# Kernel optimization log

Measured on AMD Instinct MI355X. Metric: run time of the kernel, lower is better.

The kernel has to match this reference:

```python
import jax, jax.numpy as jnp
import numpy as np

NUM_EXPERTS = 8
NUM_LANGS = 4
TOP_K = 2
D_MODEL = 1024
EXPERT_SIZE = 4096
B, S = 2, 2048


def setup_inputs() -> dict:
    key = jax.random.key(0)
    ks = jax.random.split(key, 6)
    def xavier(k, shape, fan_in, fan_out):
        a = float(np.sqrt(6.0 / (fan_in + fan_out)))
        return jax.random.uniform(k, shape, jnp.float32, -a, a)
    return {
        "x": jax.random.normal(ks[0], (B, S, D_MODEL), jnp.float32),
        "router_w": xavier(ks[1], (NUM_EXPERTS, D_MODEL), D_MODEL, NUM_EXPERTS),
        "router_b": jnp.zeros((NUM_EXPERTS,), jnp.float32),
        "lang_w": xavier(ks[2], (NUM_LANGS, D_MODEL), D_MODEL, NUM_LANGS),
        "lang_b": jnp.zeros((NUM_LANGS,), jnp.float32),
        "w1": xavier(ks[3], (NUM_EXPERTS, D_MODEL, EXPERT_SIZE), D_MODEL, EXPERT_SIZE),
        "b1": jnp.zeros((NUM_EXPERTS, EXPERT_SIZE), jnp.float32),
        "w2": xavier(ks[4], (NUM_EXPERTS, EXPERT_SIZE, D_MODEL), EXPERT_SIZE, D_MODEL),
        "b2": jnp.zeros((NUM_EXPERTS, D_MODEL), jnp.float32),
    }


def reference(x, router_w, router_b, lang_w, lang_b, w1, b1, w2, b2):
    # Language-aware routing bias
    lang_logits = x @ lang_w.T + lang_b                      # [B,S,L]
    lang_probs = jax.nn.softmax(lang_logits, axis=-1)
    # lang_probs[..., idx:idx+2].sum(-1): slice may be width 1 at the edge,
    # emulate with a zero pad column.
    lp_pad = jnp.pad(lang_probs, ((0, 0), (0, 0), (0, 1)))
    idx = jnp.arange(NUM_EXPERTS) % NUM_LANGS                # [E]
    expert_weights = lp_pad[..., idx] + lp_pad[..., idx + 1] # [B,S,E]

    router_logits = x @ router_w.T + router_b + 0.1 * expert_weights
    router_probs = jax.nn.softmax(router_logits, axis=-1)   # [B,S,E]
    top_p, top_i = jax.lax.top_k(router_probs, TOP_K)        # [B,S,K]
    top_p = top_p / top_p.sum(axis=-1, keepdims=True)

    # Dense per-expert MLP (dropout=0 / eval). torch GELU default = exact erf.
    h = jax.nn.gelu(jnp.einsum('bsd,edh->bseh', x, w1) + b1, approximate=False)
    expert_out = jnp.einsum('bseh,ehd->bsed', h, w2) + b2    # [B,S,E,D]

    sel = jnp.take_along_axis(expert_out, top_i[..., None], axis=2)  # [B,S,K,D]
    return (top_p[..., None] * sel).sum(axis=2)              # [B,S,D]
```

## Files before the change

### kernel.cpp

```cpp
#include <hip/hip_runtime.h>
#include <cstdint>
#include <cstddef>

#define T_TOK 4096
#define DM 1024
#define HS 4096
#define NE 8
#define MAXROWS 9216
#define MAXTILES 72

typedef __attribute__((ext_vector_type(8))) short short8;
typedef __attribute__((ext_vector_type(4))) float floatx4;

__device__ __forceinline__ unsigned short f2bf(float f) {
  union { float f; unsigned u; } v; v.f = f;
  unsigned r = (v.u + 0x7fffu + ((v.u >> 16) & 1u)) >> 16;
  return (unsigned short)r;
}

__device__ __forceinline__ void gload_lds16(const void* g, void* l) {
  __builtin_amdgcn_global_load_lds((const __attribute__((address_space(1))) void*)g,
                                   (__attribute__((address_space(3))) void*)l, 16, 0, 0);
}


__global__ void k_init(int* counts, int* cursor, unsigned* list) {
  int i = blockIdx.x * 256 + threadIdx.x;
  if (i < NE) { counts[i] = 0; cursor[i] = 0; }
  if (i < MAXROWS) list[i] = 0xFFFFFFFFu;
}

__global__ void k_route(const float* __restrict__ x, const float* __restrict__ rw,
                        const float* __restrict__ rb, const float* __restrict__ lw,
                        const float* __restrict__ lb, int* __restrict__ top_i,
                        float* __restrict__ top_p, int* __restrict__ counts) {
  int t = blockIdx.x * 4 + (threadIdx.x >> 6);
  int lane = threadIdx.x & 63;
  const float4* xt = (const float4*)(x + (size_t)t * DM);
  float4 xv[4];
#pragma unroll
  for (int j = 0; j < 4; j++) xv[j] = xt[lane * 4 + j];
  float dots[12];
#pragma unroll
  for (int r = 0; r < 12; r++) {
    const float4* wr = (const float4*)(r < 4 ? lw + r * DM : rw + (r - 4) * DM);
    float s = 0.f;
#pragma unroll
    for (int j = 0; j < 4; j++) {
      float4 w = wr[lane * 4 + j];
      s += xv[j].x * w.x + xv[j].y * w.y + xv[j].z * w.z + xv[j].w * w.w;
    }
#pragma unroll
    for (int o = 32; o > 0; o >>= 1) s += __shfl_xor(s, o, 64);
    dots[r] = s;
  }
  if (lane == 0) {
    float lp[4]; float m = -1e30f;
#pragma unroll
    for (int i = 0; i < 4; i++) { lp[i] = dots[i] + lb[i]; m = fmaxf(m, lp[i]); }
    float sum = 0.f;
#pragma unroll
    for (int i = 0; i < 4; i++) { lp[i] = expf(lp[i] - m); sum += lp[i]; }
#pragma unroll
    for (int i = 0; i < 4; i++) lp[i] /= sum;
    float ew[4];
    ew[0] = lp[0] + lp[1]; ew[1] = lp[1] + lp[2]; ew[2] = lp[2] + lp[3]; ew[3] = lp[3];
    float r8[8];
#pragma unroll
    for (int e = 0; e < 8; e++) r8[e] = dots[4 + e] + rb[e] + 0.1f * ew[e & 3];
    int e0 = 0;
#pragma unroll
    for (int e = 1; e < 8; e++) if (r8[e] > r8[e0]) e0 = e;
    int e1 = (e0 == 0) ? 1 : 0;
#pragma unroll
    for (int e = 0; e < 8; e++) if (e != e0 && r8[e] > r8[e1]) e1 = e;
    float tt = expf(r8[e1] - r8[e0]);
    float w0 = 1.f / (1.f + tt);
    float w1 = tt / (1.f + tt);
    top_i[t * 2] = e0; top_i[t * 2 + 1] = e1;
    top_p[t * 2] = w0; top_p[t * 2 + 1] = w1;
    atomicAdd(&counts[e0], 1); atomicAdd(&counts[e1], 1);
  }
}

__global__ void k_offsets(const int* counts, int* off) {
  if (threadIdx.x == 0) {
    int acc = 0;
    for (int e = 0; e < NE; e++) {
      off[e] = acc;
      int p = ((counts[e] + 127) >> 7) << 7;
      acc += p;
    }
    off[NE] = acc;
  }
}

__global__ void k_scatter(const int* __restrict__ top_i, const int* __restrict__ off,
                          int* cursor, unsigned* __restrict__ list) {
  int t = blockIdx.x * 256 + threadIdx.x;
  if (t >= T_TOK) return;
#pragma unroll
  for (int k = 0; k < 2; k++) {
    int e = top_i[t * 2 + k];
    int pos = atomicAdd(&cursor[e], 1);
    list[off[e] + pos] = (unsigned)(t * 2 + k);
  }
}

__global__ void k_cvt_x(const float* __restrict__ x, unsigned short* __restrict__ xb) {
  int i = blockIdx.x * 256 + threadIdx.x;
  float4 v = ((const float4*)x)[i];
  union { unsigned short us[4]; uint2 u2; } o;
  o.us[0] = f2bf(v.x); o.us[1] = f2bf(v.y); o.us[2] = f2bf(v.z); o.us[3] = f2bf(v.w);
  ((uint2*)xb)[i] = o.u2;
}

__global__ void k_transpose_bf16(const float* __restrict__ src, unsigned short* __restrict__ dst,
                                 int K, int N) {
  __shared__ float tile[64][65];
  const float* s = src + (size_t)blockIdx.z * K * N;
  unsigned short* d = dst + (size_t)blockIdx.z * K * N;
  int n0 = blockIdx.x * 64, k0 = blockIdx.y * 64;
  int tr = threadIdx.x >> 4;
  int tc = (threadIdx.x & 15) * 4;
#pragma unroll
  for (int j = 0; j < 4; j++) {
    int row = tr + j * 16;
    float4 v = *(const float4*)&s[(size_t)(k0 + row) * N + n0 + tc];
    tile[row][tc + 0] = v.x; tile[row][tc + 1] = v.y;
    tile[row][tc + 2] = v.z; tile[row][tc + 3] = v.w;
  }
  __syncthreads();
#pragma unroll
  for (int j = 0; j < 4; j++) {
    int n = tr + j * 16;
    union { unsigned short us[4]; uint2 u2; } o;
#pragma unroll
    for (int i = 0; i < 4; i++) o.us[i] = f2bf(tile[tc + i][n]);
    *(uint2*)&d[(size_t)(n0 + n) * K + k0 + tc] = o.u2;
  }
}

__global__ void k_init_out(const int* __restrict__ top_i, const float* __restrict__ top_p,
                           const float* __restrict__ b2, float* __restrict__ out) {
  int i = blockIdx.x * 256 + threadIdx.x;
  int t = i >> 10, d = i & 1023;
  int e0 = top_i[t * 2], e1 = top_i[t * 2 + 1];
  out[i] = top_p[t * 2] * b2[e0 * DM + d] + top_p[t * 2 + 1] * b2[e1 * DM + d];
}

template <int MODE>
__global__ __launch_bounds__(256, 4) void k_gemm(
    const unsigned short* __restrict__ Abase,
    const unsigned short* __restrict__ Wt,
    const int* __restrict__ off, const unsigned* __restrict__ list,
    const float* __restrict__ b1, const float* __restrict__ top_p,
    unsigned short* __restrict__ Hout, float* __restrict__ out,
    int K, int N) {
  int nx = gridDim.x;
  int flat = blockIdx.y * nx + blockIdx.x;
  int cpx = (nx * gridDim.y) >> 3;
  int swz = (flat & 7) * cpx + (flat >> 3);
  int n0 = (swz % nx) * 128;
  int r0 = (swz / nx) * 128;

  int total = off[NE];
  if (r0 >= total) return;
  int e = 0;
  while (r0 >= off[e + 1]) ++e;

  __shared__ __align__(16) unsigned short lA[2][128 * 32];
  __shared__ __align__(16) unsigned short lB[2][128 * 32];
  __shared__ float sP[128];
  __shared__ int sTok[128];

  int tid = threadIdx.x;
  int srow = tid >> 2;
  int key_s = (srow >> 1) & 3;
  int koff_src = (((tid & 3) ^ key_s) * 8);
  int kdst = (tid & 3) * 8;

  const unsigned short* srcA[2];
#pragma unroll
  for (int c = 0; c < 2; c++) {
    int row = c * 64 + srow;
    size_t arow;
    if (MODE == 0) {
      unsigned pair = list[r0 + row];
      arow = (pair == 0xFFFFFFFFu) ? 0 : (size_t)(pair >> 1);
    } else {
      arow = (size_t)(r0 + row);
    }
    srcA[c] = Abase + arow * K + koff_src;
  }
  const unsigned short* srcB[2];
#pragma unroll
  for (int c = 0; c < 2; c++)
    srcB[c] = Wt + ((size_t)e * N + n0 + c * 64 + srow) * K + koff_src;

  if (MODE == 1 && tid < 128) {
    unsigned pair = list[r0 + tid];
    if (pair == 0xFFFFFFFFu) { sTok[tid] = -1; sP[tid] = 0.f; }
    else { sTok[tid] = (int)(pair >> 1); sP[tid] = top_p[pair]; }
  }

  floatx4 acc[4][4] = {};
  int lane = tid & 63;
  int w = tid >> 6;
  int wm = w >> 1, wn = w & 1;
  int lr = lane & 15, kq = lane >> 4;
  int kx = kq ^ ((lr >> 1) & 3);

#define STAGE(BUF, KK)                                                        \
  do {                                                                        \
    _Pragma("unroll")                                                         \
    for (int c = 0; c < 2; c++) {                                             \
      gload_lds16(srcA[c] + (KK), &lA[BUF][(c * 64 + srow) * 32 + kdst]);     \
      gload_lds16(srcB[c] + (KK), &lB[BUF][(c * 64 + srow) * 32 + kdst]);     \
    }                                                                         \
  } while (0)

  STAGE(0, 0);
  __syncthreads();

  int cur = 0;
  for (int k0 = 0; k0 < K; k0 += 32) {
    if (k0 + 32 < K) STAGE(cur ^ 1, k0 + 32);
    const short8* pA = (const short8*)lA[cur];
    const short8* pB = (const short8*)lB[cur];
    short8 a[4], b[4];
#pragma unroll
    for (int i = 0; i < 4; i++) a[i] = pA[(wm * 64 + i * 16 + lr) * 4 + kx];
#pragma unroll
    for (int j = 0; j < 4; j++) b[j] = pB[(wn * 64 + j * 16 + lr) * 4 + kx];
#pragma unroll
    for (int i = 0; i < 4; i++)
#pragma unroll
      for (int j = 0; j < 4; j++)
        acc[i][j] = __builtin_amdgcn_mfma_f32_16x16x32_bf16(a[i], b[j], acc[i][j], 0, 0, 0);
    __syncthreads();
    cur ^= 1;
  }
#undef STAGE

  int rbase = wm * 64 + kq * 4;
  int cbase = wn * 64 + lr;
  if (MODE == 0) {
#pragma unroll
    for (int i = 0; i < 4; i++)
#pragma unroll
      for (int j = 0; j < 4; j++)
#pragma unroll
        for (int g = 0; g < 4; g++) {
          int row = rbase + i * 16 + g;
          int col = cbase + j * 16;
          float v = acc[i][j][g] + b1[e * HS + n0 + col];
          v = 0.5f * v * (1.f + erff(v * 0.70710678118f));
          Hout[(size_t)(r0 + row) * (size_t)N + n0 + col] = f2bf(v);
        }
  } else {
#pragma unroll
    for (int i = 0; i < 4; i++)
#pragma unroll
      for (int j = 0; j < 4; j++)
#pragma unroll
        for (int g = 0; g < 4; g++) {
          int row = rbase + i * 16 + g;
          int col = cbase + j * 16;
          int tok = sTok[row];
          if (tok >= 0)
            atomicAdd(&out[(size_t)tok * DM + n0 + col], sP[row] * acc[i][j][g]);
        }
  }
}


extern "C" void kernel_launch(void* const* d_in, const int* in_sizes, int n_in,
                              void* d_out, int out_size, void* d_ws, size_t ws_size,
                              hipStream_t stream) {
  const float* x  = (const float*)d_in[0];
  const float* rw = (const float*)d_in[1];
  const float* rb = (const float*)d_in[2];
  const float* lw = (const float*)d_in[3];
  const float* lb = (const float*)d_in[4];
  const float* w1 = (const float*)d_in[5];
  const float* b1 = (const float*)d_in[6];
  const float* w2 = (const float*)d_in[7];
  const float* b2 = (const float*)d_in[8];
  float* out = (float*)d_out;
  char* ws = (char*)d_ws;

  int* counts = (int*)ws;
  int* cursor = (int*)(ws + 32);
  int* off    = (int*)(ws + 64);
  int* top_i  = (int*)(ws + 128);
  float* top_p = (float*)(ws + 128 + 32768);
  unsigned* list = (unsigned*)(ws + 65792);
  unsigned short* xb = (unsigned short*)(ws + 102912);
  unsigned short* wt = (unsigned short*)(ws + 102912 + 8388608);
  unsigned short* h  = (unsigned short*)(ws + 102912 + 8388608 + 67108864);

  k_init<<<dim3((MAXROWS + 255) / 256), dim3(256), 0, stream>>>(counts, cursor, list);
  k_route<<<dim3(T_TOK / 4), dim3(256), 0, stream>>>(x, rw, rb, lw, lb, top_i, top_p, counts);
  k_offsets<<<dim3(1), dim3(64), 0, stream>>>(counts, off);
  k_scatter<<<dim3(T_TOK / 256), dim3(256), 0, stream>>>(top_i, off, cursor, list);
  k_cvt_x<<<dim3(T_TOK * DM / 4 / 256), dim3(256), 0, stream>>>(x, xb);
  k_transpose_bf16<<<dim3(HS / 64, DM / 64, NE), dim3(256), 0, stream>>>(w1, wt, DM, HS);
  k_gemm<0><<<dim3(HS / 128, MAXTILES), dim3(256), 0, stream>>>(
      xb, wt, off, list, b1, top_p, h, nullptr, DM, HS);
  k_transpose_bf16<<<dim3(DM / 64, HS / 64, NE), dim3(256), 0, stream>>>(w2, wt, HS, DM);
  k_init_out<<<dim3(T_TOK * DM / 256), dim3(256), 0, stream>>>(top_i, top_p, b2, out);
  k_gemm<1><<<dim3(DM / 128, MAXTILES), dim3(256), 0, stream>>>(
      h, wt, off, list, nullptr, top_p, nullptr, out, HS, DM);
}
```

Baseline: 515.4 us.

## Fuse weight transpose and bf16 conversion into GEMM B-tile loading

Removes the separate transpose-to-bf16 kernels for w1 and w2 and instead has the GEMM read fp32 weights directly, converting and packing them into the swizzled LDS layout through registers with software pipelining. K and N become template parameters. This eliminates the extra full-weight passes and workspace buffer, but B loads now go through registers and read fp32 per tile (twice the bytes, repeated across row tiles), and occupancy bounds drop from 4 to 2 blocks.

```diff
diff --git a/kernel.cpp b/kernel.cpp
--- a/kernel.cpp
+++ b/kernel.cpp
@@ -16,6 +16,10 @@
   union { float f; unsigned u; } v; v.f = f;
   unsigned r = (v.u + 0x7fffu + ((v.u >> 16) & 1u)) >> 16;
   return (unsigned short)r;
+}
+
+__device__ __forceinline__ unsigned pack2bf(float a, float b) {
+  return (unsigned)f2bf(a) | ((unsigned)f2bf(b) << 16);
 }
 
 __device__ __forceinline__ void gload_lds16(const void* g, void* l) {
@@ -115,32 +119,6 @@
   ((uint2*)xb)[i] = o.u2;
 }
 
-__global__ void k_transpose_bf16(const float* __restrict__ src, unsigned short* __restrict__ dst,
-                                 int K, int N) {
-  __shared__ float tile[64][65];
-  const float* s = src + (size_t)blockIdx.z * K * N;
-  unsigned short* d = dst + (size_t)blockIdx.z * K * N;
-  int n0 = blockIdx.x * 64, k0 = blockIdx.y * 64;
-  int tr = threadIdx.x >> 4;
-  int tc = (threadIdx.x & 15) * 4;
-#pragma unroll
-  for (int j = 0; j < 4; j++) {
-    int row = tr + j * 16;
-    float4 v = *(const float4*)&s[(size_t)(k0 + row) * N + n0 + tc];
-    tile[row][tc + 0] = v.x; tile[row][tc + 1] = v.y;
-    tile[row][tc + 2] = v.z; tile[row][tc + 3] = v.w;
-  }
-  __syncthreads();
-#pragma unroll
-  for (int j = 0; j < 4; j++) {
-    int n = tr + j * 16;
-    union { unsigned short us[4]; uint2 u2; } o;
-#pragma unroll
-    for (int i = 0; i < 4; i++) o.us[i] = f2bf(tile[tc + i][n]);
-    *(uint2*)&d[(size_t)(n0 + n) * K + k0 + tc] = o.u2;
-  }
-}
-
 __global__ void k_init_out(const int* __restrict__ top_i, const float* __restrict__ top_p,
                            const float* __restrict__ b2, float* __restrict__ out) {
   int i = blockIdx.x * 256 + threadIdx.x;
@@ -149,14 +127,13 @@
   out[i] = top_p[t * 2] * b2[e0 * DM + d] + top_p[t * 2 + 1] * b2[e1 * DM + d];
 }
 
-template <int MODE>
-__global__ __launch_bounds__(256, 4) void k_gemm(
+template <int MODE, int K, int N>
+__global__ __launch_bounds__(256, 2) void k_gemm(
     const unsigned short* __restrict__ Abase,
-    const unsigned short* __restrict__ Wt,
+    const float* __restrict__ W,
     const int* __restrict__ off, const unsigned* __restrict__ list,
-    const float* __restrict__ b1, const float* __restrict__ top_p,
-    unsigned short* __restrict__ Hout, float* __restrict__ out,
-    int K, int N) {
+    const float* __restrict__ bias, const float* __restrict__ top_p,
+    unsigned short* __restrict__ Hout, float* __restrict__ out) {
   int nx = gridDim.x;
   int flat = blockIdx.y * nx + blockIdx.x;
   int cpx = (nx * gridDim.y) >> 3;
@@ -177,7 +154,7 @@
   int tid = threadIdx.x;
   int srow = tid >> 2;
   int key_s = (srow >> 1) & 3;
-  int koff_src = (((tid & 3) ^ key_s) * 8);
+  int koff_src = ((tid & 3) ^ key_s) * 8;
   int kdst = (tid & 3) * 8;
 
   const unsigned short* srcA[2];
@@ -193,10 +170,11 @@
     }
     srcA[c] = Abase + arow * K + koff_src;
   }
-  const unsigned short* srcB[2];
-#pragma unroll
-  for (int c = 0; c < 2; c++)
-    srcB[c] = Wt + ((size_t)e * N + n0 + c * 64 + srow) * K + koff_src;
+
+  int bq = tid >> 6;
+  int bn = (tid & 63) * 2;
+  const float* pB = W + (size_t)e * K * N + (size_t)(bq * 8) * N + n0 + bn;
+  int pc = (bq ^ ((bn >> 1) & 3)) * 8;
 
   if (MODE == 1 && tid < 128) {
     unsigned pair = list[r0 + tid];
@@ -211,37 +189,63 @@
   int lr = lane & 15, kq = lane >> 4;
   int kx = kq ^ ((lr >> 1) & 3);
 
-#define STAGE(BUF, KK)                                                        \
+  float2 rb[8];
+
+#define ALOAD(BUF, KK)                                                        \
   do {                                                                        \
     _Pragma("unroll")                                                         \
-    for (int c = 0; c < 2; c++) {                                             \
+    for (int c = 0; c < 2; c++)                                               \
       gload_lds16(srcA[c] + (KK), &lA[BUF][(c * 64 + srow) * 32 + kdst]);     \
-      gload_lds16(srcB[c] + (KK), &lB[BUF][(c * 64 + srow) * 32 + kdst]);     \
-    }                                                                         \
   } while (0)
 
-  STAGE(0, 0);
+#define BLOAD(KK)                                                             \
+  do {                                                                        \
+    const float* p_ = pB + (size_t)(KK) * N;                                  \
+    _Pragma("unroll")                                                         \
+    for (int j = 0; j < 8; j++) rb[j] = *(const float2*)(p_ + (size_t)j * N); \
+  } while (0)
+
+#define BWRITE(BUF)                                                           \
+  do {                                                                        \
+    uint4 q0, q1;                                                             \
+    q0.x = pack2bf(rb[0].x, rb[1].x); q0.y = pack2bf(rb[2].x, rb[3].x);       \
+    q0.z = pack2bf(rb[4].x, rb[5].x); q0.w = pack2bf(rb[6].x, rb[7].x);       \
+    q1.x = pack2bf(rb[0].y, rb[1].y); q1.y = pack2bf(rb[2].y, rb[3].y);       \
+    q1.z = pack2bf(rb[4].y, rb[5].y); q1.w = pack2bf(rb[6].y, rb[7].y);       \
+    *(uint4*)&lB[BUF][bn * 32 + pc] = q0;                                     \
+    *(uint4*)&lB[BUF][(bn + 1) * 32 + pc] = q1;                               \
+  } while (0)
+
+  ALOAD(0, 0);
+  BLOAD(0);
+  BWRITE(0);
   __syncthreads();
 
   int cur = 0;
   for (int k0 = 0; k0 < K; k0 += 32) {
-    if (k0 + 32 < K) STAGE(cur ^ 1, k0 + 32);
-    const short8* pA = (const short8*)lA[cur];
-    const short8* pB = (const short8*)lB[cur];
+    if (k0 + 32 < K) {
+      ALOAD(cur ^ 1, k0 + 32);
+      BLOAD(k0 + 32);
+    }
+    const short8* pAf = (const short8*)lA[cur];
+    const short8* pBf = (const short8*)lB[cur];
     short8 a[4], b[4];
 #pragma unroll
-    for (int i = 0; i < 4; i++) a[i] = pA[(wm * 64 + i * 16 + lr) * 4 + kx];
-#pragma unroll
-    for (int j = 0; j < 4; j++) b[j] = pB[(wn * 64 + j * 16 + lr) * 4 + kx];
+    for (int i = 0; i < 4; i++) a[i] = pAf[(wm * 64 + i * 16 + lr) * 4 + kx];
+#pragma unroll
+    for (int j = 0; j < 4; j++) b[j] = pBf[(wn * 64 + j * 16 + lr) * 4 + kx];
 #pragma unroll
     for (int i = 0; i < 4; i++)
 #pragma unroll
       for (int j = 0; j < 4; j++)
         acc[i][j] = __builtin_amdgcn_mfma_f32_16x16x32_bf16(a[i], b[j], acc[i][j], 0, 0, 0);
+    if (k0 + 32 < K) BWRITE(cur ^ 1);
     __syncthreads();
     cur ^= 1;
   }
-#undef STAGE
+#undef ALOAD
+#undef BLOAD
+#undef BWRITE
 
   int rbase = wm * 64 + kq * 4;
   int cbase = wn * 64 + lr;
@@ -254,7 +258,7 @@
         for (int g = 0; g < 4; g++) {
           int row = rbase + i * 16 + g;
           int col = cbase + j * 16;
-          float v = acc[i][j][g] + b1[e * HS + n0 + col];
+          float v = acc[i][j][g] + bias[e * N + n0 + col];
           v = 0.5f * v * (1.f + erff(v * 0.70710678118f));
           Hout[(size_t)(r0 + row) * (size_t)N + n0 + col] = f2bf(v);
         }
@@ -297,19 +301,16 @@
   float* top_p = (float*)(ws + 128 + 32768);
   unsigned* list = (unsigned*)(ws + 65792);
   unsigned short* xb = (unsigned short*)(ws + 102912);
-  unsigned short* wt = (unsigned short*)(ws + 102912 + 8388608);
-  unsigned short* h  = (unsigned short*)(ws + 102912 + 8388608 + 67108864);
+  unsigned short* h  = (unsigned short*)(ws + 102912 + 8388608);
 
   k_init<<<dim3((MAXROWS + 255) / 256), dim3(256), 0, stream>>>(counts, cursor, list);
   k_route<<<dim3(T_TOK / 4), dim3(256), 0, stream>>>(x, rw, rb, lw, lb, top_i, top_p, counts);
   k_offsets<<<dim3(1), dim3(64), 0, stream>>>(counts, off);
   k_scatter<<<dim3(T_TOK / 256), dim3(256), 0, stream>>>(top_i, off, cursor, list);
   k_cvt_x<<<dim3(T_TOK * DM / 4 / 256), dim3(256), 0, stream>>>(x, xb);
-  k_transpose_bf16<<<dim3(HS / 64, DM / 64, NE), dim3(256), 0, stream>>>(w1, wt, DM, HS);
-  k_gemm<0><<<dim3(HS / 128, MAXTILES), dim3(256), 0, stream>>>(
-      xb, wt, off, list, b1, top_p, h, nullptr, DM, HS);
-  k_transpose_bf16<<<dim3(DM / 64, HS / 64, NE), dim3(256), 0, stream>>>(w2, wt, HS, DM);
   k_init_out<<<dim3(T_TOK * DM / 256), dim3(256), 0, stream>>>(top_i, top_p, b2, out);
-  k_gemm<1><<<dim3(DM / 128, MAXTILES), dim3(256), 0, stream>>>(
-      h, wt, off, list, nullptr, top_p, nullptr, out, HS, DM);
-}
+  k_gemm<0, DM, HS><<<dim3(HS / 128, MAXTILES), dim3(256), 0, stream>>>(
+      xb, w1, off, list, b1, top_p, h, nullptr);
+  k_gemm<1, HS, DM><<<dim3(DM / 128, MAXTILES), dim3(256), 0, stream>>>(
+      h, w2, off, list, nullptr, top_p, nullptr, out);
+}
```

After: 549.0 us. 1.07x slower.
